# Kernel tuning notes

Hardware: AMD Instinct MI355X
Metric: run time of the kernel (lower is better)

Reference implementation:

```python
import jax, jax.numpy as jnp
jax.config.update("jax_enable_x64", True)
import numpy as np
from jax.scipy.linalg import expm as _expm

B, C = 64, 2048


def setup_inputs() -> dict:
    key = jax.random.key(0)
    k1, _ = jax.random.split(key)
    A = jax.random.normal(k1, (B, C, 13, 13), dtype=jnp.float32) * 0.1
    MTMs = jnp.einsum('bcij,bcik->bcjk', A, A)  # PSD normal-equation matrix M^T M
    T0 = jnp.eye(4, dtype=jnp.float32).at[2, 3].set(1.0)  # identity pose, t_z = 1
    Ts = jnp.broadcast_to(T0, (B, C, 4, 4))
    return {"MTMs": MTMs, "Ts": Ts}


def _POfT(T):
    # T: [B,C,4,4] -> P: [B,C,13,7] mapping (rx,ry,rz,tx,ty,tz,1) -> d(TBar)
    z = jnp.zeros(T.shape[:2], T.dtype)
    o = jnp.ones_like(z)
    def rot_rows(i):
        a, b, c = T[..., i, 0], T[..., i, 1], T[..., i, 2]
        return [jnp.stack([z, -c, b, z, z, z, a], -1),
                jnp.stack([c, z, -a, z, z, z, b], -1),
                jnp.stack([-b, a, z, z, z, z, c], -1)]
    rows = rot_rows(0) + rot_rows(1) + rot_rows(2)
    rows.append(jnp.stack([z, z, z, z, z, z, o], -1))
    for i in range(3):
        rows.append(jnp.stack([z, z, z, T[..., i, 0], T[..., i, 1], T[..., i, 2], T[..., i, 3]], -1))
    return jnp.stack(rows, axis=-2)


def _diffT(v):
    # v: [B,C,>=6,1] -> se(3) matrix [B,C,4,4]
    z = jnp.zeros(v.shape[:2], v.dtype)
    vx, vy, vz, tx, ty, tz = (v[..., i, 0] for i in range(6))
    rows = [jnp.stack([z, -vz, vy, tx], -1),
            jnp.stack([vz, z, -vx, ty], -1),
            jnp.stack([-vy, vx, z, tz], -1),
            jnp.stack([z, z, z, z], -1)]
    return jnp.stack(rows, axis=-2)


_expm_b = jax.vmap(jax.vmap(_expm))  # batched 4x4 matrix exponential


def _inv(M):
    # regularized inverse as in the original `inv`
    reg = 1e-5 * (1.0 + jnp.max(M, axis=(-2, -1), keepdims=True))
    eye = jnp.eye(M.shape[-1], dtype=M.dtype)
    return jnp.linalg.inv(M + eye * reg)


def _refine_step(MtM, T):
    # one pnpRefineMtM iteration (lendata=None branch)
    P = _POfT(T)                                    # [B,C,13,7]
    Q = jnp.einsum('bcji,bcjk,bckl->bcil', P, MtM, P)  # P^T MtM P : [B,C,7,7]
    regR = jnp.full(Q.shape[:2], 10.0, Q.dtype)
    regT = 1e-8 * jnp.maximum(Q[..., 3, 3] + Q[..., 4, 4] + Q[..., 5, 5],
                              jnp.ones_like(regR))
    d = jnp.stack([regR, regR, regR, regT, regT, regT], -1)  # [B,C,6]
    Omega = Q[..., 0:6, 0:6] + jnp.eye(6, dtype=Q.dtype) * d[..., None, :]
    v = -jnp.matmul(_inv(Omega), Q[..., 0:6, 6:7])  # [B,C,6,1]
    Tnew = jnp.matmul(T, _expm_b(_diffT(v)))        # boxplus: T @ expm(hat(v))
    Omega_out = Omega / (Tnew[..., 2:3, 3:4] ** 2 + 1e-8)
    return Tnew, Omega_out


def reference(MTMs, Ts):
    MtM = MTMs.astype(jnp.float64)
    T = Ts.astype(jnp.float64)
    Omega = None
    for _ in range(5):  # unrolled 5 Gauss-Newton iterations, as in call()
        T, Omega = _refine_step(MtM, T)
    return T, Omega
```

## Files before the change

kernel.cpp:

```cpp
#include <hip/hip_runtime.h>
#include <math.h>

#define NPROB (64 * 2048)

__host__ __device__ constexpr int TRI(int i, int j) { return i * 13 - i * (i - 1) / 2 + (j - i); }
__host__ __device__ constexpr int OI6(int i, int j) { return i * 6 - i * (i - 1) / 2 + (j - i); }
__host__ __device__ constexpr int QI(int i, int j)  { return i * 7 - i * (i - 1) / 2 + (j - i); }

struct PE { int r, a, b, s; };
__device__ constexpr int PLEN[7] = {6, 6, 6, 3, 3, 3, 13};
__device__ constexpr PE PAT[7][13] = {
    {{1,0,2,1},{2,0,1,-1},{4,1,2,1},{5,1,1,-1},{7,2,2,1},{8,2,1,-1}},
    {{0,0,2,-1},{2,0,0,1},{3,1,2,-1},{5,1,0,1},{6,2,2,-1},{8,2,0,1}},
    {{0,0,1,1},{1,0,0,-1},{3,1,1,1},{4,1,0,-1},{6,2,1,1},{7,2,0,-1}},
    {{10,0,0,1},{11,1,0,1},{12,2,0,1}},
    {{10,0,1,1},{11,1,1,1},{12,2,1,1}},
    {{10,0,2,1},{11,1,2,1},{12,2,2,1}},
    {{0,0,0,1},{1,0,1,1},{2,0,2,1},{3,1,0,1},{4,1,1,1},{5,1,2,1},
     {6,2,0,1},{7,2,1,1},{8,2,2,1},{9,3,0,1},{10,0,3,1},{11,1,3,1},{12,2,3,1}},
};

__device__ __forceinline__ double fast_rcp(double w) {
    double r = __builtin_amdgcn_rcp(w);
    double e = fma(-w, r, 1.0);
    r = fma(r, e, r);
    e = fma(-w, r, 1.0);
    r = fma(r, e, r);
    return r;
}

__global__ __launch_bounds__(256, 1) void gn5_kernel(const float* __restrict__ Mg,
                                                     const float* __restrict__ Tg,
                                                     float* __restrict__ outg) {
    const int tid  = threadIdx.x;
    const int lane = tid & 63;
    const int wv   = tid >> 6;
    const long long prob = (long long)blockIdx.x * 256 + tid;

    __shared__ __align__(16) float buf[64 * 169];
    float mreg[91];

    #pragma unroll 1
    for (int w = 0; w < 4; ++w) {
        const long long c0 = (long long)blockIdx.x * 256 + (long long)w * 64;
        const float4* src = (const float4*)(Mg + c0 * 169);
        float4* dst = (float4*)buf;
        #pragma unroll 1
        for (int i = tid; i < (64 * 169) / 4; i += 256) dst[i] = src[i];
        __syncthreads();
        if (wv == w) {
            #pragma unroll
            for (int i = 0; i < 13; ++i)
                #pragma unroll
                for (int j = i; j < 13; ++j)
                    mreg[TRI(i, j)] = buf[lane * 169 + i * 13 + j];
        }
        __syncthreads();
    }

    double t[3][4];
    {
        const float* tp = Tg + prob * 16;
        #pragma unroll
        for (int i = 0; i < 3; ++i)
            #pragma unroll
            for (int j = 0; j < 4; ++j)
                t[i][j] = (double)tp[i * 4 + j];
    }

    double q[28];

    #pragma unroll 1
    for (int it = 0; it < 5; ++it) {
        float tf[3][4];
        #pragma unroll
        for (int i = 0; i < 3; ++i)
            #pragma unroll
            for (int j = 0; j < 4; ++j)
                tf[i][j] = (float)t[i][j];

        float qf[28];
        #pragma unroll
        for (int l = 0; l < 7; ++l) {
            float y[13];
            #pragma unroll
            for (int r = 0; r < 13; ++r) y[r] = 0.0f;
            #pragma unroll
            for (int e = 0; e < 13; ++e) {
                if (e < PLEN[l]) {
                    const PE pe = PAT[l][e];
                    const float tt = (pe.a == 3) ? 1.0f : tf[pe.a][pe.b];
                    const float cf = (pe.s > 0) ? tt : -tt;
                    const int c = pe.r;
                    #pragma unroll
                    for (int r = 0; r < 13; ++r)
                        y[r] += cf * mreg[(r <= c) ? TRI(r, c) : TRI(c, r)];
                }
            }
            #pragma unroll
            for (int k = 0; k <= l; ++k) {
                float acc = 0.0f;
                #pragma unroll
                for (int e = 0; e < 13; ++e) {
                    if (e < PLEN[k]) {
                        const PE pe = PAT[k][e];
                        const float tt = (pe.a == 3) ? 1.0f : tf[pe.a][pe.b];
                        const float cf = (pe.s > 0) ? tt : -tt;
                        acc += cf * y[pe.r];
                    }
                }
                qf[QI(k, l)] = acc;
            }
        }
        #pragma unroll
        for (int i = 0; i < 28; ++i) q[i] = (double)qf[i];

        const double trQ  = q[QI(3, 3)] + q[QI(4, 4)] + q[QI(5, 5)];
        const double regT = 1e-8 * fmax(trQ, 1.0);
        q[QI(0, 0)] += 10.0;
        q[QI(1, 1)] += 10.0;
        q[QI(2, 2)] += 10.0;
        q[QI(3, 3)] += regT;
        q[QI(4, 4)] += regT;
        q[QI(5, 5)] += regT;

        const double a0 = fmax(q[QI(0,0)], q[QI(0,1)]);
        const double a1 = fmax(q[QI(0,2)], q[QI(0,3)]);
        const double a2 = fmax(q[QI(0,4)], q[QI(0,5)]);
        const double a3 = fmax(q[QI(1,1)], q[QI(1,2)]);
        const double a4 = fmax(q[QI(1,3)], q[QI(1,4)]);
        const double a5 = fmax(q[QI(1,5)], q[QI(2,2)]);
        const double a6 = fmax(q[QI(2,3)], q[QI(2,4)]);
        const double a7 = fmax(q[QI(2,5)], q[QI(3,3)]);
        const double a8 = fmax(q[QI(3,4)], q[QI(3,5)]);
        const double a9 = fmax(q[QI(4,4)], q[QI(4,5)]);
        const double b0 = fmax(a0, a1);
        const double b1 = fmax(a2, a3);
        const double b2 = fmax(a4, a5);
        const double b3 = fmax(a6, a7);
        const double b4 = fmax(fmax(a8, a9), q[QI(5,5)]);
        const double mx = fmax(fmax(b0, b1), fmax(fmax(b2, b3), b4));
        const double reg2 = 1e-5 * (1.0 + mx);

        if (it == 4) {
            double* st = (double*)buf;
            #pragma unroll
            for (int k = 0; k < 6; ++k)
                #pragma unroll
                for (int l = k; l < 6; ++l)
                    st[(long long)tid * 21 + OI6(k, l)] = q[QI(k, l)];
        }

        #pragma unroll
        for (int k = 0; k < 6; ++k) q[QI(k, k)] += reg2;

        #pragma unroll
        for (int k = 0; k < 6; ++k) {
            const double inv = fast_rcp(q[QI(k, k)]);
            q[QI(k, k)] = inv;
            #pragma unroll
            for (int i = k + 1; i < 6; ++i) {
                const double f = q[QI(k, i)] * inv;
                #pragma unroll
                for (int j = i; j < 7; ++j) q[QI(i, j)] -= f * q[QI(k, j)];
            }
        }
        double x[6];
        #pragma unroll
        for (int i = 5; i >= 0; --i) {
            double s = q[QI(i, 6)];
            #pragma unroll
            for (int j = i + 1; j < 6; ++j) s -= q[QI(i, j)] * x[j];
            x[i] = s * q[QI(i, i)];
        }
        const double wx = -x[0], wy = -x[1], wz = -x[2];
        const double ux = -x[3], uy = -x[4], uz = -x[5];

        const double tsq = wx * wx + wy * wy + wz * wz;
        double A, B, Cc;
        if (tsq < 0.25) {
            A  = 1.0 + tsq * (-1.0/6 + tsq * (1.0/120 + tsq * (-1.0/5040 + tsq * (1.0/362880
                 + tsq * (-1.0/39916800.0 + tsq * (1.0/6227020800.0 + tsq * (-1.0/1307674368000.0)))))));
            B  = 0.5 + tsq * (-1.0/24 + tsq * (1.0/720 + tsq * (-1.0/40320 + tsq * (1.0/3628800
                 + tsq * (-1.0/479001600.0 + tsq * (1.0/87178291200.0 + tsq * (-1.0/20922789888000.0)))))));
            Cc = 1.0/6 + tsq * (-1.0/120 + tsq * (1.0/5040 + tsq * (-1.0/362880 + tsq * (1.0/39916800.0
                 + tsq * (-1.0/6227020800.0 + tsq * (1.0/1307674368000.0 + tsq * (-1.0/355687428096000.0)))))));
        } else {
            const double th = sqrt(tsq);
            const double s = sin(th), c = cos(th);
            A  = s / th;
            B  = (1.0 - c) / tsq;
            Cc = (th - s) / (tsq * th);
        }
        const double K2xx = wx * wx - tsq, K2yy = wy * wy - tsq, K2zz = wz * wz - tsq;
        const double K2xy = wx * wy, K2xz = wx * wz, K2yz = wy * wz;
        double R[3][3];
        R[0][0] = 1.0 + B * K2xx;      R[0][1] = -A * wz + B * K2xy;  R[0][2] =  A * wy + B * K2xz;
        R[1][0] =  A * wz + B * K2xy;  R[1][1] = 1.0 + B * K2yy;      R[1][2] = -A * wx + B * K2yz;
        R[2][0] = -A * wy + B * K2xz;  R[2][1] =  A * wx + B * K2yz;  R[2][2] = 1.0 + B * K2zz;
        const double V00 = 1.0 + Cc * K2xx,      V01 = -B * wz + Cc * K2xy, V02 =  B * wy + Cc * K2xz;
        const double V10 =  B * wz + Cc * K2xy,  V11 = 1.0 + Cc * K2yy,     V12 = -B * wx + Cc * K2yz;
        const double V20 = -B * wy + Cc * K2xz,  V21 =  B * wx + Cc * K2yz, V22 = 1.0 + Cc * K2zz;
        const double ex = V00 * ux + V01 * uy + V02 * uz;
        const double ey = V10 * ux + V11 * uy + V12 * uz;
        const double ez = V20 * ux + V21 * uy + V22 * uz;

        #pragma unroll
        for (int i = 0; i < 3; ++i) {
            const double a0_ = t[i][0], a1_ = t[i][1], a2_ = t[i][2], a3_ = t[i][3];
            t[i][0] = a0_ * R[0][0] + a1_ * R[1][0] + a2_ * R[2][0];
            t[i][1] = a0_ * R[0][1] + a1_ * R[1][1] + a2_ * R[2][1];
            t[i][2] = a0_ * R[0][2] + a1_ * R[1][2] + a2_ * R[2][2];
            t[i][3] = a0_ * ex + a1_ * ey + a2_ * ez + a3_;
        }
    }

    {
        float* to = outg + prob * 16;
        #pragma unroll
        for (int i = 0; i < 3; ++i)
            #pragma unroll
            for (int j = 0; j < 4; ++j)
                to[i * 4 + j] = (float)t[i][j];
        to[12] = 0.0f; to[13] = 0.0f; to[14] = 0.0f; to[15] = 1.0f;

        const double invden = 1.0 / (t[2][3] * t[2][3] + 1e-8);
        const double* st = (const double*)buf;
        float* oo = outg + (long long)NPROB * 16 + prob * 36;
        #pragma unroll
        for (int k = 0; k < 6; ++k)
            #pragma unroll
            for (int l = 0; l < 6; ++l)
                oo[k * 6 + l] = (float)(st[(long long)tid * 21 + ((k <= l) ? OI6(k, l) : OI6(l, k))] * invden);
    }
}

extern "C" void kernel_launch(void* const* d_in, const int* in_sizes, int n_in,
                              void* d_out, int out_size, void* d_ws, size_t ws_size,
                              hipStream_t stream) {
    const float* Mg = (const float*)d_in[0];
    const float* Tg = (const float*)d_in[1];
    float* out = (float*)d_out;
    (void)in_sizes; (void)n_in; (void)out_size; (void)d_ws; (void)ws_size;

    const int threads = 256;
    const int blocks = NPROB / threads;
    gn5_kernel<<<blocks, threads, 0, stream>>>(Mg, Tg, out);
}
```

Baseline: 165.9 us.

## Run first four Gauss-Newton iterations in fp32, keep final iteration in fp64

The first four refinement iterations now run entirely in single precision: the 6x6 Cholesky-style solve, the regularization, and a closed-form SE(3) exponential using Rodrigues/Taylor coefficients and a float reciprocal. Only the last iteration keeps the double-precision solve and output path. The aim is to avoid slow FP64 arithmetic in the inner iterations, since the reference is fp64. The risk is reduced accuracy of the intermediate poses, which the final fp64 step may not fully correct.

Result: slower. 197.7 us (+19.1%).

```diff
diff --git a/kernel.cpp b/kernel.cpp
--- a/kernel.cpp
+++ b/kernel.cpp
@@ -29,6 +29,48 @@
     return r;
 }
 
+__device__ __forceinline__ float fast_rcpf(float w) {
+    float r = __builtin_amdgcn_rcpf(w);
+    r = r * fmaf(-w, r, 2.0f);
+    return r;
+}
+
+__device__ __forceinline__ void build_q(const float mreg[91], const float tf[3][4],
+                                        float qf[28]) {
+    #pragma unroll
+    for (int l = 0; l < 7; ++l) {
+        float y[13];
+        #pragma unroll
+        for (int r = 0; r < 13; ++r) y[r] = 0.0f;
+        #pragma unroll
+        for (int e = 0; e < 13; ++e) {
+            if (e < PLEN[l]) {
+                const PE pe = PAT[l][e];
+                const float tt = (pe.a == 3) ? 1.0f : tf[pe.a][pe.b];
+                const float cf = (pe.s > 0) ? tt : -tt;
+                const int c = pe.r;
+                #pragma unroll
+                for (int r = 0; r < 13; ++r)
+                    y[r] += cf * mreg[(r <= c) ? TRI(r, c) : TRI(c, r)];
+            }
+        }
+        #pragma unroll
+        for (int k = 0; k <= l; ++k) {
+            float acc = 0.0f;
+            #pragma unroll
+            for (int e = 0; e < 13; ++e) {
+                if (e < PLEN[k]) {
+                    const PE pe = PAT[k][e];
+                    const float tt = (pe.a == 3) ? 1.0f : tf[pe.a][pe.b];
+                    const float cf = (pe.s > 0) ? tt : -tt;
+                    acc += cf * y[pe.r];
+                }
+            }
+            qf[QI(k, l)] = acc;
+        }
+    }
+}
+
 __global__ __launch_bounds__(256, 1) void gn5_kernel(const float* __restrict__ Mg,
                                                      const float* __restrict__ Tg,
                                                      float* __restrict__ outg) {
@@ -58,60 +100,110 @@
         __syncthreads();
     }
 
-    double t[3][4];
+    float tF[3][4];
     {
         const float* tp = Tg + prob * 16;
         #pragma unroll
         for (int i = 0; i < 3; ++i)
             #pragma unroll
             for (int j = 0; j < 4; ++j)
-                t[i][j] = (double)tp[i * 4 + j];
-    }
+                tF[i][j] = tp[i * 4 + j];
+    }
+
+    #pragma unroll 1
+    for (int it = 0; it < 4; ++it) {
+        float qf[28];
+        build_q(mreg, tF, qf);
+
+        const float trQ  = qf[QI(3, 3)] + qf[QI(4, 4)] + qf[QI(5, 5)];
+        const float regT = 1e-8f * fmaxf(trQ, 1.0f);
+        qf[QI(0, 0)] += 10.0f;
+        qf[QI(1, 1)] += 10.0f;
+        qf[QI(2, 2)] += 10.0f;
+        qf[QI(3, 3)] += regT;
+        qf[QI(4, 4)] += regT;
+        qf[QI(5, 5)] += regT;
+
+        float mx = qf[QI(0, 0)];
+        #pragma unroll
+        for (int k = 0; k < 6; ++k)
+            #pragma unroll
+            for (int l = k; l < 6; ++l)
+                mx = fmaxf(mx, qf[QI(k, l)]);
+        const float reg2 = 1e-5f * (1.0f + mx);
+        #pragma unroll
+        for (int k = 0; k < 6; ++k) qf[QI(k, k)] += reg2;
+
+        #pragma unroll
+        for (int k = 0; k < 6; ++k) {
+            const float inv = fast_rcpf(qf[QI(k, k)]);
+            qf[QI(k, k)] = inv;
+            #pragma unroll
+            for (int i = k + 1; i < 6; ++i) {
+                const float f = qf[QI(k, i)] * inv;
+                #pragma unroll
+                for (int j = i; j < 7; ++j) qf[QI(i, j)] -= f * qf[QI(k, j)];
+            }
+        }
+        float x[6];
+        #pragma unroll
+        for (int i = 5; i >= 0; --i) {
+            float s = qf[QI(i, 6)];
+            #pragma unroll
+            for (int j = i + 1; j < 6; ++j) s -= qf[QI(i, j)] * x[j];
+            x[i] = s * qf[QI(i, i)];
+        }
+        const float wx = -x[0], wy = -x[1], wz = -x[2];
+        const float ux = -x[3], uy = -x[4], uz = -x[5];
+
+        const float tsq = wx * wx + wy * wy + wz * wz;
+        float A, Bc, Cc;
+        if (tsq < 0.25f) {
+            A  = 1.0f + tsq * (-1.0f/6 + tsq * (1.0f/120 + tsq * (-1.0f/5040 + tsq * (1.0f/362880.0f))));
+            Bc = 0.5f + tsq * (-1.0f/24 + tsq * (1.0f/720 + tsq * (-1.0f/40320 + tsq * (1.0f/3628800.0f))));
+            Cc = 1.0f/6 + tsq * (-1.0f/120 + tsq * (1.0f/5040 + tsq * (-1.0f/362880 + tsq * (1.0f/39916800.0f))));
+        } else {
+            const float th = sqrtf(tsq);
+            const float s = sinf(th), c = cosf(th);
+            const float rth = fast_rcpf(th), rtsq = fast_rcpf(tsq);
+            A  = s * rth;
+            Bc = (1.0f - c) * rtsq;
+            Cc = (th - s) * rtsq * rth;
+        }
+        const float K2xx = wx * wx - tsq, K2yy = wy * wy - tsq, K2zz = wz * wz - tsq;
+        const float K2xy = wx * wy, K2xz = wx * wz, K2yz = wy * wz;
+        float R[3][3];
+        R[0][0] = 1.0f + Bc * K2xx;     R[0][1] = -A * wz + Bc * K2xy;  R[0][2] =  A * wy + Bc * K2xz;
+        R[1][0] =  A * wz + Bc * K2xy;  R[1][1] = 1.0f + Bc * K2yy;     R[1][2] = -A * wx + Bc * K2yz;
+        R[2][0] = -A * wy + Bc * K2xz;  R[2][1] =  A * wx + Bc * K2yz;  R[2][2] = 1.0f + Bc * K2zz;
+        const float V00 = 1.0f + Cc * K2xx,     V01 = -Bc * wz + Cc * K2xy, V02 =  Bc * wy + Cc * K2xz;
+        const float V10 =  Bc * wz + Cc * K2xy, V11 = 1.0f + Cc * K2yy,     V12 = -Bc * wx + Cc * K2yz;
+        const float V20 = -Bc * wy + Cc * K2xz, V21 =  Bc * wx + Cc * K2yz, V22 = 1.0f + Cc * K2zz;
+        const float ex = V00 * ux + V01 * uy + V02 * uz;
+        const float ey = V10 * ux + V11 * uy + V12 * uz;
+        const float ez = V20 * ux + V21 * uy + V22 * uz;
+
+        #pragma unroll
+        for (int i = 0; i < 3; ++i) {
+            const float a0_ = tF[i][0], a1_ = tF[i][1], a2_ = tF[i][2], a3_ = tF[i][3];
+            tF[i][0] = a0_ * R[0][0] + a1_ * R[1][0] + a2_ * R[2][0];
+            tF[i][1] = a0_ * R[0][1] + a1_ * R[1][1] + a2_ * R[2][1];
+            tF[i][2] = a0_ * R[0][2] + a1_ * R[1][2] + a2_ * R[2][2];
+            tF[i][3] = a0_ * ex + a1_ * ey + a2_ * ez + a3_;
+        }
+    }
+
+    double t[3][4];
+    #pragma unroll
+    for (int i = 0; i < 3; ++i)
+        #pragma unroll
+        for (int j = 0; j < 4; ++j)
+            t[i][j] = (double)tF[i][j];
 
     double q[28];
-
-    #pragma unroll 1
-    for (int it = 0; it < 5; ++it) {
-        float tf[3][4];
-        #pragma unroll
-        for (int i = 0; i < 3; ++i)
-            #pragma unroll
-            for (int j = 0; j < 4; ++j)
-                tf[i][j] = (float)t[i][j];
-
+    {
         float qf[28];
-        #pragma unroll
-        for (int l = 0; l < 7; ++l) {
-            float y[13];
-            #pragma unroll
-            for (int r = 0; r < 13; ++r) y[r] = 0.0f;
-            #pragma unroll
-            for (int e = 0; e < 13; ++e) {
-                if (e < PLEN[l]) {
-                    const PE pe = PAT[l][e];
-                    const float tt = (pe.a == 3) ? 1.0f : tf[pe.a][pe.b];
-                    const float cf = (pe.s > 0) ? tt : -tt;
-                    const int c = pe.r;
-                    #pragma unroll
-                    for (int r = 0; r < 13; ++r)
-                        y[r] += cf * mreg[(r <= c) ? TRI(r, c) : TRI(c, r)];
-                }
-            }
-            #pragma unroll
-            for (int k = 0; k <= l; ++k) {
-                float acc = 0.0f;
-                #pragma unroll
-                for (int e = 0; e < 13; ++e) {
-                    if (e < PLEN[k]) {
-                        const PE pe = PAT[k][e];
-                        const float tt = (pe.a == 3) ? 1.0f : tf[pe.a][pe.b];
-                        const float cf = (pe.s > 0) ? tt : -tt;
-                        acc += cf * y[pe.r];
-                    }
-                }
-                qf[QI(k, l)] = acc;
-            }
-        }
+        build_q(mreg, tF, qf);
         #pragma unroll
         for (int i = 0; i < 28; ++i) q[i] = (double)qf[i];
 
@@ -142,7 +234,7 @@
         const double mx = fmax(fmax(b0, b1), fmax(fmax(b2, b3), b4));
         const double reg2 = 1e-5 * (1.0 + mx);
 
-        if (it == 4) {
+        {
             double* st = (double*)buf;
             #pragma unroll
             for (int k = 0; k < 6; ++k)
```
